# Kernel optimization log

Measured on AMD Instinct MI355X. Metric: run time of the kernel, lower is better.

## Reference

```python
import jax, jax.numpy as jnp
import numpy as np

# Contiguous token segment lengths per group (static, sums to 4096)
LEN_GROUPS = (256, 512, 768, 384, 640, 512, 576, 448)
NUM_GROUPS, D_IN, D_OUT = 8, 512, 512
BATCH = 16


def setup_inputs() -> dict:
    key = jax.random.key(0)
    k1, k2, k3 = jax.random.split(key, 3)
    T = int(sum(LEN_GROUPS))
    x = jax.random.normal(k1, (BATCH, T, D_IN), dtype=jnp.float32)
    # nn.Linear default init: U(-1/sqrt(fan_in), 1/sqrt(fan_in))
    bound = 1.0 / np.sqrt(D_IN)
    W = jax.random.uniform(k2, (NUM_GROUPS, D_OUT, D_IN), jnp.float32, -bound, bound)
    b = jax.random.uniform(k3, (NUM_GROUPS, D_OUT), jnp.float32, -bound, bound)
    return {"x": x, "W": W, "b": b}


def reference(x, W, b):
    # Per-group Linear over contiguous token segments, then concat along tokens.
    # Loop is over a small static group count; segment bounds are Python ints,
    # so slicing is static and jit-compatible.
    outs = []
    start = 0
    for i, L in enumerate(LEN_GROUPS):
        seg = x[:, start:start + L]                     # [B, L, D_in]
        outs.append(jnp.einsum('btd,od->bto', seg, W[i]) + b[i])  # [B, L, D_out]
        start += L
    return jnp.concatenate(outs, axis=1)               # [B, T, D_out]
```

## Files before the change

### kernel.cpp

```cpp
#include <hip/hip_runtime.h>
#include <hip/hip_bf16.h>
#include <cstdint>

#define BATCH 16
#define TTOT  4096
#define DIN   512
#define DOUT  512
#define NG    8
#define NJOB  33
#define NKT   16

typedef float f32x4 __attribute__((ext_vector_type(4)));
typedef short s16x8 __attribute__((ext_vector_type(8)));

__device__ __forceinline__ short f2b(float f) {
    union { __bf16 b; short s; } u; u.b = (__bf16)f; return u.s;
}

__device__ __constant__ short JT0[NJOB] = {
    0,128, 256,384,512,640, 768,896,1024,1152,1280,1408, 1536,1664,1792,
    1920,2048,2176,2304,2432, 2560,2688,2816,2944, 3072,3200,3328,3456,
    3584, 3648, 3712,3840,3968};
__device__ __constant__ char JG[NJOB] = {
    0,0, 1,1,1,1, 2,2,2,2,2,2, 3,3,3, 4,4,4,4,4, 5,5,5,5, 6,6,6,6, 6, 7, 7,7,7};
__device__ __constant__ char JBM[NJOB] = {
    127,127, 127,127,127,127, 127,127,127,127,127,127, 127,127,127,
    127,127,127,127,127, 127,127,127,127, 127,127,127,127, 63, 63, 127,127,127};

__global__ void wconv_kernel(const float* __restrict__ W, ushort* __restrict__ wbf) {
    int gid = blockIdx.x * 256 + threadIdx.x;
    int c = gid >> 9;
    int q = (gid & 511) << 4;
    int r = q >> 6;
    int slot = (q >> 4) & 3;
    int kt = c & 15, nt = (c >> 4) & 3, g = c >> 6;
    int k = (kt << 5) + (((slot ^ ((r >> 1) & 3))) << 3);
    const float* wp = W + ((size_t)((g << 9) + (nt << 7) + r) << 9) + k;
    float4 v0 = *reinterpret_cast<const float4*>(wp);
    float4 v1 = *reinterpret_cast<const float4*>(wp + 4);
    s16x8 o;
    o[0]=f2b(v0.x); o[1]=f2b(v0.y); o[2]=f2b(v0.z); o[3]=f2b(v0.w);
    o[4]=f2b(v1.x); o[5]=f2b(v1.y); o[6]=f2b(v1.z); o[7]=f2b(v1.w);
    *reinterpret_cast<s16x8*>((char*)wbf + (size_t)c * 8192 + q) = o;
}

__launch_bounds__(256, 4)
__global__ void gemm_kernel(const float* __restrict__ x,
                            const ushort* __restrict__ wbf,
                            const float* __restrict__ bias,
                            float* __restrict__ out) {
    __shared__ __align__(16) char smem[32768];

    const int tid  = threadIdx.x;
    const int lane = tid & 63;
    const int wv   = tid >> 6;
    const int wm   = wv >> 1;
    const int wn   = wv & 1;
    const int colf = lane & 15;
    const int kg   = lane >> 4;

    const int p    = blockIdx.x;
    const int l    = (p & 7) * 264 + (p >> 3);
    const int nt   = l & 3;
    const int rest = l >> 2;
    const int job  = rest >> 4;
    const int bb   = rest & 15;
    const int t0   = JT0[job];
    const int g    = JG[job];
    const int bmm1 = JBM[job];
    const int n0   = nt << 7;

    const char* bchunk = (const char*)wbf + ((size_t)(((g << 2) + nt) << 4)) * 8192;

    const int r = tid >> 1;
    const int h = tid & 1;
    const int re = (r <= bmm1) ? r : bmm1;
    const float* aptr = x + ((size_t)(bb * TTOT + t0 + re) << 9) + (h << 4);
    const int sr = (r >> 1) & 3;
    const int aw0 = (r << 6) + ((((h << 1) | 0) ^ sr) << 4);
    const int aw1 = (r << 6) + ((((h << 1) | 1) ^ sr) << 4);

    float4 aE[4], aO[4];

#define ISSUE_A(S, KT_) do {                                                \
        const float* p_ = aptr + ((KT_) << 5);                              \
        a##S[0] = *(const float4*)(p_);                                     \
        a##S[1] = *(const float4*)(p_ + 4);                                 \
        a##S[2] = *(const float4*)(p_ + 8);                                 \
        a##S[3] = *(const float4*)(p_ + 12);                                \
    } while (0)

#define CVT_WRITE_A(S, KT_) do {                                            \
        char* ab_ = smem + (((KT_) & 1) << 13);                             \
        s16x8 o0_, o1_;                                                     \
        o0_[0]=f2b(a##S[0].x); o0_[1]=f2b(a##S[0].y);                       \
        o0_[2]=f2b(a##S[0].z); o0_[3]=f2b(a##S[0].w);                       \
        o0_[4]=f2b(a##S[1].x); o0_[5]=f2b(a##S[1].y);                       \
        o0_[6]=f2b(a##S[1].z); o0_[7]=f2b(a##S[1].w);                       \
        o1_[0]=f2b(a##S[2].x); o1_[1]=f2b(a##S[2].y);                       \
        o1_[2]=f2b(a##S[2].z); o1_[3]=f2b(a##S[2].w);                       \
        o1_[4]=f2b(a##S[3].x); o1_[5]=f2b(a##S[3].y);                       \
        o1_[6]=f2b(a##S[3].z); o1_[7]=f2b(a##S[3].w);                       \
        *(s16x8*)(ab_ + aw0) = o0_;                                         \
        *(s16x8*)(ab_ + aw1) = o1_;                                         \
    } while (0)

#define ISSUE_B(KT_) do {                                                   \
        const char* s_ = bchunk + ((size_t)(KT_) << 13) + tid * 16;         \
        char* d_ = smem + 16384 + (((KT_) & 1) << 13) + tid * 16;           \
        __builtin_amdgcn_global_load_lds(                                   \
            (const __attribute__((address_space(1))) void*)(s_),            \
            (__attribute__((address_space(3))) void*)(d_), 16, 0, 0);       \
        __builtin_amdgcn_global_load_lds(                                   \
            (const __attribute__((address_space(1))) void*)(s_ + 4096),     \
            (__attribute__((address_space(3))) void*)(d_ + 4096), 16, 0, 0);\
    } while (0)

#define COMPUTE(KT_) do {                                                   \
        const char* ab_ = smem + (((KT_) & 1) << 13);                       \
        const char* bb_ = smem + 16384 + (((KT_) & 1) << 13);               \
        __builtin_amdgcn_s_setprio(1);                                      \
        s16x8 bf[4];                                                        \
        _Pragma("unroll")                                                   \
        for (int ni = 0; ni < 4; ++ni) {                                    \
            int r_ = wn * 64 + ni * 16 + colf;                              \
            bf[ni] = *(const s16x8*)(bb_ + (r_ << 6)                        \
                        + (((kg ^ ((r_ >> 1) & 3))) << 4));                 \
        }                                                                   \
        _Pragma("unroll")                                                   \
        for (int mi = 0; mi < 4; ++mi) {                                    \
            int r_ = wm * 64 + mi * 16 + colf;                              \
            s16x8 af = *(const s16x8*)(ab_ + (r_ << 6)                      \
                        + (((kg ^ ((r_ >> 1) & 3))) << 4));                 \
            _Pragma("unroll")                                               \
            for (int ni = 0; ni < 4; ++ni)                                  \
                acc[mi][ni] = __builtin_amdgcn_mfma_f32_16x16x32_bf16(      \
                    af, bf[ni], acc[mi][ni], 0, 0, 0);                      \
        }                                                                   \
        __builtin_amdgcn_s_setprio(0);                                      \
    } while (0)

#define FENCE  asm volatile("" ::: "memory")
#define WAITV4 asm volatile("s_waitcnt vmcnt(4)" ::: "memory")
#define WAITV0 asm volatile("s_waitcnt vmcnt(0)" ::: "memory")
#define WAITL0 asm volatile("s_waitcnt lgkmcnt(0)" ::: "memory")
#define BAR    __builtin_amdgcn_s_barrier()

    f32x4 acc[4][4];
#pragma unroll
    for (int mi = 0; mi < 4; ++mi)
#pragma unroll
        for (int ni = 0; ni < 4; ++ni)
            acc[mi][ni] = (f32x4){0.f, 0.f, 0.f, 0.f};

    ISSUE_A(E, 0);
    FENCE;
    ISSUE_B(0);
    FENCE;
    ISSUE_A(O, 1);
    FENCE;
    CVT_WRITE_A(E, 0);
    WAITV4;
    WAITL0;
    BAR;

#pragma unroll
    for (int kt = 0; kt < NKT; ++kt) {
        if (kt + 1 < NKT) { ISSUE_B(kt + 1); FENCE; }
        if (kt + 2 < NKT) {
            if (((kt + 2) & 1) == 0) { ISSUE_A(E, kt + 2); }
            else                     { ISSUE_A(O, kt + 2); }
            FENCE;
        }
        COMPUTE(kt);
        if (kt + 1 < NKT) {
            if (((kt + 1) & 1) == 0) { CVT_WRITE_A(E, kt + 1); }
            else                     { CVT_WRITE_A(O, kt + 1); }
            if (kt + 2 < NKT) { WAITV4; }
            else              { WAITV0; }
            WAITL0;
            BAR;
        }
    }
    BAR;

    float* cbuf = (float*)smem;
    const int er = tid >> 3;
    const int ec = (tid & 7) << 4;
    float4 bvv[4];
#pragma unroll
    for (int i = 0; i < 4; ++i)
        bvv[i] = *(const float4*)(bias + (g << 9) + n0 + ec + (i << 2));

#pragma unroll
    for (int pp = 0; pp < 4; ++pp) {
        if (wm == (pp >> 1)) {
#pragma unroll
            for (int m = 0; m < 2; ++m) {
                const int mi = (pp & 1) * 2 + m;
#pragma unroll
                for (int ni = 0; ni < 4; ++ni) {
                    const int base = (m * 16 + kg * 4) * 132 + wn * 64 + ni * 16 + colf;
                    f32x4 v = acc[mi][ni];
                    cbuf[base]       = v[0];
                    cbuf[base + 132] = v[1];
                    cbuf[base + 264] = v[2];
                    cbuf[base + 396] = v[3];
                }
            }
        }
        WAITL0;
        BAR;
        const int row = pp * 32 + er;
        if (row <= bmm1) {
            float* orow = out + ((size_t)(bb * TTOT + t0 + row) << 9) + n0 + ec;
            const float* crow = cbuf + er * 132 + ec;
#pragma unroll
            for (int i = 0; i < 4; ++i) {
                float4 v = *(const float4*)(crow + (i << 2));
                float4 o4;
                o4.x = v.x + bvv[i].x; o4.y = v.y + bvv[i].y;
                o4.z = v.z + bvv[i].z; o4.w = v.w + bvv[i].w;
                *(float4*)(orow + (i << 2)) = o4;
            }
        }
        BAR;
    }
#undef ISSUE_A
#undef CVT_WRITE_A
#undef ISSUE_B
#undef COMPUTE
#undef FENCE
#undef WAITV4
#undef WAITV0
#undef WAITL0
#undef BAR
}

__launch_bounds__(256)
__global__ void gemm_fallback(const float* __restrict__ x,
                              const float* __restrict__ W,
                              const float* __restrict__ bias,
                              float* __restrict__ out) {
    __shared__ __align__(16) char smem[49152];
    const int tid  = threadIdx.x;
    const int lane = tid & 63;
    const int wid  = tid >> 6;
    const int wm   = wid >> 1;
    const int wn   = wid & 1;
    const int p  = blockIdx.x;
    const int l  = ((p & 7) << 9) + (p >> 3);
    const int mt = l >> 2;
    const int nt = l & 3;
    const int bb = mt >> 6;
    const int t0 = (mt & 63) << 6;
    const int n0 = nt << 7;
    int g = 0;
    if (t0 >= 256)  g++; if (t0 >= 768)  g++; if (t0 >= 1536) g++;
    if (t0 >= 1920) g++; if (t0 >= 2560) g++; if (t0 >= 3072) g++;
    if (t0 >= 3648) g++;
    const int arow = tid >> 2;
    const int acol = (tid & 3) << 4;
    const float* aptr = x + ((size_t)(bb * TTOT + t0 + arow)) * DIN + acol;
    float4 a0, a1, a2, a3;
    float4 bw0[4], bw1[4];
    auto load_global = [&](int k0) {
        a0 = *(const float4*)(aptr + k0);
        a1 = *(const float4*)(aptr + k0 + 4);
        a2 = *(const float4*)(aptr + k0 + 8);
        a3 = *(const float4*)(aptr + k0 + 12);
#pragma unroll
        for (int pp = 0; pp < 4; ++pp) {
            int idx = pp * 256 + tid;
            int row = idx >> 3, seg = idx & 7;
            const float* wp = W + ((size_t)((g << 9) + n0 + row)) * DIN + k0 + (seg << 3);
            bw0[pp] = *(const float4*)(wp);
            bw1[pp] = *(const float4*)(wp + 4);
        }
    };
    auto swzf = [](int row, int bc) { return (row << 7) + (bc ^ ((row & 7) << 4)); };
    auto write_lds = [&](int buf) {
        char* ab  = smem + buf * 8192;
        char* bb_ = smem + 16384 + buf * 16384;
        s16x8 w0, w1;
        w0[0]=f2b(a0.x); w0[1]=f2b(a0.y); w0[2]=f2b(a0.z); w0[3]=f2b(a0.w);
        w0[4]=f2b(a1.x); w0[5]=f2b(a1.y); w0[6]=f2b(a1.z); w0[7]=f2b(a1.w);
        w1[0]=f2b(a2.x); w1[1]=f2b(a2.y); w1[2]=f2b(a2.z); w1[3]=f2b(a2.w);
        w1[4]=f2b(a3.x); w1[5]=f2b(a3.y); w1[6]=f2b(a3.z); w1[7]=f2b(a3.w);
        const int abase2 = acol << 1;
        *(s16x8*)(ab + swzf(arow, abase2))      = w0;
        *(s16x8*)(ab + swzf(arow, abase2 + 16)) = w1;
#pragma unroll
        for (int pp = 0; pp < 4; ++pp) {
            int idx = pp * 256 + tid;
            int row = idx >> 3, seg = idx & 7;
            s16x8 wvv;
            wvv[0]=f2b(bw0[pp].x); wvv[1]=f2b(bw0[pp].y);
            wvv[2]=f2b(bw0[pp].z); wvv[3]=f2b(bw0[pp].w);
            wvv[4]=f2b(bw1[pp].x); wvv[5]=f2b(bw1[pp].y);
            wvv[6]=f2b(bw1[pp].z); wvv[7]=f2b(bw1[pp].w);
            *(s16x8*)(bb_ + swzf(row, seg << 4)) = wvv;
        }
    };
    f32x4 acc[2][4];
#pragma unroll
    for (int mi = 0; mi < 2; ++mi)
#pragma unroll
        for (int ni = 0; ni < 4; ++ni) acc[mi][ni] = (f32x4){0.f,0.f,0.f,0.f};
    const int colf = lane & 15;
    const int kgrp = lane >> 4;
    auto compute = [&](int buf) {
        const char* ab  = smem + buf * 8192;
        const char* bb_ = smem + 16384 + buf * 16384;
#pragma unroll
        for (int ks = 0; ks < 2; ++ks) {
            const int kb = ks * 64 + kgrp * 16;
            s16x8 af[2], bf[4];
#pragma unroll
            for (int mi = 0; mi < 2; ++mi)
                af[mi] = *(const s16x8*)(ab + swzf(wm * 32 + mi * 16 + colf, kb));
#pragma unroll
            for (int ni = 0; ni < 4; ++ni)
                bf[ni] = *(const s16x8*)(bb_ + swzf(wn * 64 + ni * 16 + colf, kb));
#pragma unroll
            for (int mi = 0; mi < 2; ++mi)
#pragma unroll
                for (int ni = 0; ni < 4; ++ni)
                    acc[mi][ni] = __builtin_amdgcn_mfma_f32_16x16x32_bf16(
                        af[mi], bf[ni], acc[mi][ni], 0, 0, 0);
        }
    };
    load_global(0);
    write_lds(0);
    __syncthreads();
    int buf = 0;
#pragma unroll 1
    for (int kt = 0; kt < 8; ++kt) {
        if (kt < 7) load_global((kt + 1) << 6);
        compute(buf);
        if (kt < 7) write_lds(buf ^ 1);
        __syncthreads();
        buf ^= 1;
    }
    float* cbuf = (float*)smem;
#pragma unroll
    for (int ni = 0; ni < 4; ++ni) {
        const int c = wn * 64 + ni * 16 + colf;
#pragma unroll
        for (int mi = 0; mi < 2; ++mi) {
            const int rr2 = wm * 32 + mi * 16 + kgrp * 4;
            f32x4 v = acc[mi][ni];
            cbuf[(rr2 + 0) * 132 + c] = v[0];
            cbuf[(rr2 + 1) * 132 + c] = v[1];
            cbuf[(rr2 + 2) * 132 + c] = v[2];
            cbuf[(rr2 + 3) * 132 + c] = v[3];
        }
    }
    __syncthreads();
    const int rr = tid >> 5;
    const int cc = (tid & 31) << 2;
    const float4 bvv = *(const float4*)(bias + (g << 9) + n0 + cc);
#pragma unroll
    for (int it = 0; it < 8; ++it) {
        const int row = it * 8 + rr;
        float4 v = *(const float4*)(cbuf + row * 132 + cc);
        float4 o4; o4.x = v.x + bvv.x; o4.y = v.y + bvv.y;
                   o4.z = v.z + bvv.z; o4.w = v.w + bvv.w;
        *(float4*)(out + ((size_t)(bb * TTOT) + t0 + row) * DOUT + n0 + cc) = o4;
    }
}

extern "C" void kernel_launch(void* const* d_in, const int* in_sizes, int n_in,
                              void* d_out, int out_size, void* d_ws, size_t ws_size,
                              hipStream_t stream) {
    const float* x    = (const float*)d_in[0];
    const float* W    = (const float*)d_in[1];
    const float* bias = (const float*)d_in[2];
    float* out = (float*)d_out;

    const size_t wbytes = (size_t)NG * DOUT * DIN * sizeof(ushort);

    if (ws_size >= wbytes) {
        ushort* wbf = (ushort*)d_ws;
        wconv_kernel<<<1024, 256, 0, stream>>>(W, wbf);
        gemm_kernel<<<NJOB * BATCH * 4, 256, 0, stream>>>(x, wbf, bias, out);
    } else {
        gemm_fallback<<<BATCH * 64 * 4, 256, 0, stream>>>(x, W, bias, out);
    }
}
```

Measured before the change: 117.0 us.

## Load pre-swizzled weight fragments straight into registers and double the K tile

The weight conversion now writes bf16 W in MFMA fragment order, so each wave loads its B operands straight from global memory into registers instead of staging them through LDS with global_load_lds. The K tile doubles to 64, halving the number of k-steps and barriers. The A tile gets a new 128-byte-row XOR swizzle in a 32 KB double buffer. The aim is to free LDS bandwidth and cut synchronisation, at the cost of more live registers, so launch bounds drop to 2 blocks per CU and latency hiding may suffer.

New measurement: 102.5 us. -12.4%, faster.

```diff
diff --git a/kernel.cpp b/kernel.cpp
--- a/kernel.cpp
+++ b/kernel.cpp
@@ -8,7 +8,7 @@
 #define DOUT  512
 #define NG    8
 #define NJOB  33
-#define NKT   16
+#define NKT   8
 
 typedef float f32x4 __attribute__((ext_vector_type(4)));
 typedef short s16x8 __attribute__((ext_vector_type(8)));
@@ -29,22 +29,26 @@
 
 __global__ void wconv_kernel(const float* __restrict__ W, ushort* __restrict__ wbf) {
     int gid = blockIdx.x * 256 + threadIdx.x;
-    int c = gid >> 9;
-    int q = (gid & 511) << 4;
-    int r = q >> 6;
-    int slot = (q >> 4) & 3;
-    int kt = c & 15, nt = (c >> 4) & 3, g = c >> 6;
-    int k = (kt << 5) + (((slot ^ ((r >> 1) & 3))) << 3);
-    const float* wp = W + ((size_t)((g << 9) + (nt << 7) + r) << 9) + k;
+    int l  = gid & 63;
+    int u  = gid >> 6;
+    int ks = u & 1;
+    int ni = (u >> 1) & 3;
+    int wn = (u >> 3) & 1;
+    int kt = (u >> 4) & 7;
+    int nt = (u >> 7) & 3;
+    int g  = u >> 9;
+    int row = nt * 128 + wn * 64 + ni * 16 + (l & 15);
+    int k   = kt * 64 + ks * 32 + (l >> 4) * 8;
+    const float* wp = W + ((size_t)(g * DOUT + row)) * DIN + k;
     float4 v0 = *reinterpret_cast<const float4*>(wp);
     float4 v1 = *reinterpret_cast<const float4*>(wp + 4);
     s16x8 o;
     o[0]=f2b(v0.x); o[1]=f2b(v0.y); o[2]=f2b(v0.z); o[3]=f2b(v0.w);
     o[4]=f2b(v1.x); o[5]=f2b(v1.y); o[6]=f2b(v1.z); o[7]=f2b(v1.w);
-    *reinterpret_cast<s16x8*>((char*)wbf + (size_t)c * 8192 + q) = o;
-}
-
-__launch_bounds__(256, 4)
+    *reinterpret_cast<s16x8*>((char*)wbf + (size_t)gid * 16) = o;
+}
+
+__launch_bounds__(256, 2)
 __global__ void gemm_kernel(const float* __restrict__ x,
                             const ushort* __restrict__ wbf,
                             const float* __restrict__ bias,
@@ -70,79 +74,67 @@
     const int bmm1 = JBM[job];
     const int n0   = nt << 7;
 
-    const char* bchunk = (const char*)wbf + ((size_t)(((g << 2) + nt) << 4)) * 8192;
-
-    const int r = tid >> 1;
-    const int h = tid & 1;
-    const int re = (r <= bmm1) ? r : bmm1;
-    const float* aptr = x + ((size_t)(bb * TTOT + t0 + re) << 9) + (h << 4);
-    const int sr = (r >> 1) & 3;
-    const int aw0 = (r << 6) + ((((h << 1) | 0) ^ sr) << 4);
-    const int aw1 = (r << 6) + ((((h << 1) | 1) ^ sr) << 4);
-
-    float4 aE[4], aO[4];
+    const char* bfbase = (const char*)wbf
+        + ((size_t)((g * 4 + nt) * 8)) * 16384 + (wn ? 8192 : 0) + lane * 16;
+
+    const int arow_s = (wv << 5) + (lane >> 3);
+    const int col8   = (lane & 7) << 3;
+    const float* aptr = x + ((size_t)(bb * TTOT + t0 + arow_s)) * DIN + col8;
+
+    float4 stE[4][2], stO[4][2];
+    s16x8 bE[8], bO[8];
 
 #define ISSUE_A(S, KT_) do {                                                \
-        const float* p_ = aptr + ((KT_) << 5);                              \
-        a##S[0] = *(const float4*)(p_);                                     \
-        a##S[1] = *(const float4*)(p_ + 4);                                 \
-        a##S[2] = *(const float4*)(p_ + 8);                                 \
-        a##S[3] = *(const float4*)(p_ + 12);                                \
+        _Pragma("unroll")                                                   \
+        for (int j_ = 0; j_ < 4; ++j_) {                                    \
+            const float* p_ = aptr + (size_t)(j_ * 8) * DIN + ((KT_) << 6); \
+            st##S[j_][0] = *(const float4*)(p_);                            \
+            st##S[j_][1] = *(const float4*)(p_ + 4);                        \
+        }                                                                   \
     } while (0)
 
 #define CVT_WRITE_A(S, KT_) do {                                            \
-        char* ab_ = smem + (((KT_) & 1) << 13);                             \
-        s16x8 o0_, o1_;                                                     \
-        o0_[0]=f2b(a##S[0].x); o0_[1]=f2b(a##S[0].y);                       \
-        o0_[2]=f2b(a##S[0].z); o0_[3]=f2b(a##S[0].w);                       \
-        o0_[4]=f2b(a##S[1].x); o0_[5]=f2b(a##S[1].y);                       \
-        o0_[6]=f2b(a##S[1].z); o0_[7]=f2b(a##S[1].w);                       \
-        o1_[0]=f2b(a##S[2].x); o1_[1]=f2b(a##S[2].y);                       \
-        o1_[2]=f2b(a##S[2].z); o1_[3]=f2b(a##S[2].w);                       \
-        o1_[4]=f2b(a##S[3].x); o1_[5]=f2b(a##S[3].y);                       \
-        o1_[6]=f2b(a##S[3].z); o1_[7]=f2b(a##S[3].w);                       \
-        *(s16x8*)(ab_ + aw0) = o0_;                                         \
-        *(s16x8*)(ab_ + aw1) = o1_;                                         \
+        char* ab_ = smem + (((KT_) & 1) << 14);                             \
+        _Pragma("unroll")                                                   \
+        for (int j_ = 0; j_ < 4; ++j_) {                                    \
+            float4 lo_ = st##S[j_][0], hi_ = st##S[j_][1];                  \
+            s16x8 o_;                                                       \
+            o_[0]=f2b(lo_.x); o_[1]=f2b(lo_.y); o_[2]=f2b(lo_.z); o_[3]=f2b(lo_.w); \
+            o_[4]=f2b(hi_.x); o_[5]=f2b(hi_.y); o_[6]=f2b(hi_.z); o_[7]=f2b(hi_.w); \
+            int row_ = arow_s + j_ * 8;                                     \
+            int bc_ = (col8 << 1) ^ ((row_ & 7) << 4);                      \
+            *(s16x8*)(ab_ + (row_ << 7) + bc_) = o_;                        \
+        }                                                                   \
     } while (0)
 
-#define ISSUE_B(KT_) do {                                                   \
-        const char* s_ = bchunk + ((size_t)(KT_) << 13) + tid * 16;         \
-        char* d_ = smem + 16384 + (((KT_) & 1) << 13) + tid * 16;           \
-        __builtin_amdgcn_global_load_lds(                                   \
-            (const __attribute__((address_space(1))) void*)(s_),            \
-            (__attribute__((address_space(3))) void*)(d_), 16, 0, 0);       \
-        __builtin_amdgcn_global_load_lds(                                   \
-            (const __attribute__((address_space(1))) void*)(s_ + 4096),     \
-            (__attribute__((address_space(3))) void*)(d_ + 4096), 16, 0, 0);\
+#define ISSUE_BF(S, KT_) do {                                               \
+        const char* b_ = bfbase + ((size_t)(KT_) << 14);                    \
+        _Pragma("unroll")                                                   \
+        for (int q_ = 0; q_ < 8; ++q_)                                      \
+            b##S[q_] = *(const s16x8*)(b_ + q_ * 1024);                     \
     } while (0)
 
-#define COMPUTE(KT_) do {                                                   \
-        const char* ab_ = smem + (((KT_) & 1) << 13);                       \
-        const char* bb_ = smem + 16384 + (((KT_) & 1) << 13);               \
-        __builtin_amdgcn_s_setprio(1);                                      \
-        s16x8 bf[4];                                                        \
+#define COMPUTE(S, KT_) do {                                                \
+        const char* ab_ = smem + (((KT_) & 1) << 14);                       \
         _Pragma("unroll")                                                   \
-        for (int ni = 0; ni < 4; ++ni) {                                    \
-            int r_ = wn * 64 + ni * 16 + colf;                              \
-            bf[ni] = *(const s16x8*)(bb_ + (r_ << 6)                        \
-                        + (((kg ^ ((r_ >> 1) & 3))) << 4));                 \
+        for (int ks = 0; ks < 2; ++ks) {                                    \
+            const int kb = ks * 64 + (kg << 4);                             \
+            s16x8 af[4];                                                    \
+            _Pragma("unroll")                                               \
+            for (int mi = 0; mi < 4; ++mi) {                                \
+                int r_ = wm * 64 + mi * 16 + colf;                          \
+                af[mi] = *(const s16x8*)(ab_ + (r_ << 7) + (kb ^ ((r_ & 7) << 4))); \
+            }                                                               \
+            _Pragma("unroll")                                               \
+            for (int mi = 0; mi < 4; ++mi)                                  \
+                _Pragma("unroll")                                           \
+                for (int ni = 0; ni < 4; ++ni)                              \
+                    acc[mi][ni] = __builtin_amdgcn_mfma_f32_16x16x32_bf16(  \
+                        af[mi], b##S[ni * 2 + ks], acc[mi][ni], 0, 0, 0);   \
         }                                                                   \
-        _Pragma("unroll")                                                   \
-        for (int mi = 0; mi < 4; ++mi) {                                    \
-            int r_ = wm * 64 + mi * 16 + colf;                              \
-            s16x8 af = *(const s16x8*)(ab_ + (r_ << 6)                      \
-                        + (((kg ^ ((r_ >> 1) & 3))) << 4));                 \
-            _Pragma("unroll")                                               \
-            for (int ni = 0; ni < 4; ++ni)                                  \
-                acc[mi][ni] = __builtin_amdgcn_mfma_f32_16x16x32_bf16(      \
-                    af, bf[ni], acc[mi][ni], 0, 0, 0);                      \
-        }                                                                   \
-        __builtin_amdgcn_s_setprio(0);                                      \
     } while (0)
 
 #define FENCE  asm volatile("" ::: "memory")
-#define WAITV4 asm volatile("s_waitcnt vmcnt(4)" ::: "memory")
-#define WAITV0 asm volatile("s_waitcnt vmcnt(0)" ::: "memory")
 #define WAITL0 asm volatile("s_waitcnt lgkmcnt(0)" ::: "memory")
 #define BAR    __builtin_amdgcn_s_barrier()
 
@@ -153,31 +145,31 @@
         for (int ni = 0; ni < 4; ++ni)
             acc[mi][ni] = (f32x4){0.f, 0.f, 0.f, 0.f};
 
+    ISSUE_BF(E, 0);
     ISSUE_A(E, 0);
-    FENCE;
-    ISSUE_B(0);
     FENCE;
     ISSUE_A(O, 1);
     FENCE;
     CVT_WRITE_A(E, 0);
-    WAITV4;
     WAITL0;
     BAR;
 
 #pragma unroll
     for (int kt = 0; kt < NKT; ++kt) {
-        if (kt + 1 < NKT) { ISSUE_B(kt + 1); FENCE; }
+        if (kt + 1 < NKT) {
+            if (((kt + 1) & 1) == 0) { ISSUE_BF(E, kt + 1); }
+            else                     { ISSUE_BF(O, kt + 1); }
+            FENCE;
+        }
         if (kt + 2 < NKT) {
             if (((kt + 2) & 1) == 0) { ISSUE_A(E, kt + 2); }
             else                     { ISSUE_A(O, kt + 2); }
             FENCE;
         }
-        COMPUTE(kt);
+        if ((kt & 1) == 0) { COMPUTE(E, kt); } else { COMPUTE(O, kt); }
         if (kt + 1 < NKT) {
             if (((kt + 1) & 1) == 0) { CVT_WRITE_A(E, kt + 1); }
             else                     { CVT_WRITE_A(O, kt + 1); }
-            if (kt + 2 < NKT) { WAITV4; }
-            else              { WAITV0; }
             WAITL0;
             BAR;
         }
@@ -213,7 +205,7 @@
         BAR;
         const int row = pp * 32 + er;
         if (row <= bmm1) {
-            float* orow = out + ((size_t)(bb * TTOT + t0 + row) << 9) + n0 + ec;
+            float* orow = out + ((size_t)(bb * TTOT + t0 + row)) * DOUT + n0 + ec;
             const float* crow = cbuf + er * 132 + ec;
 #pragma unroll
             for (int i = 0; i < 4; ++i) {
@@ -228,11 +220,9 @@
     }
 #undef ISSUE_A
 #undef CVT_WRITE_A
-#undef ISSUE_B
+#undef ISSUE_BF
 #undef COMPUTE
 #undef FENCE
-#undef WAITV4
-#undef WAITV0
 #undef WAITL0
 #undef BAR
 }
```

## Load fp32 A tiles directly into LDS and use three-stage async pipeline

Applied to the files above, without the earlier changes.

A tiles are now loaded as fp32 straight into LDS with global_load_lds instead of going through registers and a bf16 conversion before the LDS write. Conversion to bf16 moves into the compute step, applied when fragments are read from LDS. The double buffer becomes a three-slot ring, prefetching two stages ahead with vmcnt(6). This removes register staging and the per-iteration LDS write and lgkm wait. In exchange LDS grows to 72KB, occupancy bounds drop from 4 to 2 blocks, and A-tile LDS traffic doubles because the data stays fp32.

Result: faster. 101.4 us (-13.3%).

```diff
diff --git a/kernel.cpp b/kernel.cpp
--- a/kernel.cpp
+++ b/kernel.cpp
@@ -44,12 +44,12 @@
     *reinterpret_cast<s16x8*>((char*)wbf + (size_t)c * 8192 + q) = o;
 }
 
-__launch_bounds__(256, 4)
+__launch_bounds__(256, 2)
 __global__ void gemm_kernel(const float* __restrict__ x,
                             const ushort* __restrict__ wbf,
                             const float* __restrict__ bias,
                             float* __restrict__ out) {
-    __shared__ __align__(16) char smem[32768];
+    __shared__ __align__(16) char smem[73728];
 
     const int tid  = threadIdx.x;
     const int lane = tid & 63;
@@ -72,76 +72,70 @@
 
     const char* bchunk = (const char*)wbf + ((size_t)(((g << 2) + nt) << 4)) * 8192;
 
-    const int r = tid >> 1;
-    const int h = tid & 1;
-    const int re = (r <= bmm1) ? r : bmm1;
-    const float* aptr = x + ((size_t)(bb * TTOT + t0 + re) << 9) + (h << 4);
-    const int sr = (r >> 1) & 3;
-    const int aw0 = (r << 6) + ((((h << 1) | 0) ^ sr) << 4);
-    const int aw1 = (r << 6) + ((((h << 1) | 1) ^ sr) << 4);
-
-    float4 aE[4], aO[4];
-
-#define ISSUE_A(S, KT_) do {                                                \
-        const float* p_ = aptr + ((KT_) << 5);                              \
-        a##S[0] = *(const float4*)(p_);                                     \
-        a##S[1] = *(const float4*)(p_ + 4);                                 \
-        a##S[2] = *(const float4*)(p_ + 8);                                 \
-        a##S[3] = *(const float4*)(p_ + 12);                                \
+    const int srcslot = ((tid & 7) ^ ((tid >> 3) & 7)) << 4;
+    const char* pA0; const char* pA1; const char* pA2; const char* pA3;
+    {
+        int r0 = (tid >> 3);
+        int r1 = 32 + r0, r2 = 64 + r0, r3 = 96 + r0;
+        if (r2 > bmm1) r2 -= 64;
+        if (r3 > bmm1) r3 -= 64;
+        const char* xb = (const char*)(x + ((size_t)(bb * TTOT + t0)) * DIN);
+        pA0 = xb + (size_t)r0 * 2048 + srcslot;
+        pA1 = xb + (size_t)r1 * 2048 + srcslot;
+        pA2 = xb + (size_t)r2 * 2048 + srcslot;
+        pA3 = xb + (size_t)r3 * 2048 + srcslot;
+    }
+
+#define GLD(SRC_, DST_)                                                     \
+    __builtin_amdgcn_global_load_lds(                                       \
+        (const __attribute__((address_space(1))) void*)(SRC_),              \
+        (__attribute__((address_space(3))) void*)(DST_), 16, 0, 0)
+
+#define STAGE(KT_, SL_) do {                                                \
+        char* sb_ = smem + (SL_) * 24576;                                   \
+        GLD(pA0 + (KT_) * 128, sb_ + tid * 16);                             \
+        GLD(pA1 + (KT_) * 128, sb_ + 4096  + tid * 16);                     \
+        GLD(pA2 + (KT_) * 128, sb_ + 8192  + tid * 16);                     \
+        GLD(pA3 + (KT_) * 128, sb_ + 12288 + tid * 16);                     \
+        const char* bs_ = bchunk + (size_t)(KT_) * 8192 + tid * 16;         \
+        GLD(bs_,        sb_ + 16384 + tid * 16);                            \
+        GLD(bs_ + 4096, sb_ + 20480 + tid * 16);                            \
     } while (0)
 
-#define CVT_WRITE_A(S, KT_) do {                                            \
-        char* ab_ = smem + (((KT_) & 1) << 13);                             \
-        s16x8 o0_, o1_;                                                     \
-        o0_[0]=f2b(a##S[0].x); o0_[1]=f2b(a##S[0].y);                       \
-        o0_[2]=f2b(a##S[0].z); o0_[3]=f2b(a##S[0].w);                       \
-        o0_[4]=f2b(a##S[1].x); o0_[5]=f2b(a##S[1].y);                       \
-        o0_[6]=f2b(a##S[1].z); o0_[7]=f2b(a##S[1].w);                       \
-        o1_[0]=f2b(a##S[2].x); o1_[1]=f2b(a##S[2].y);                       \
-        o1_[2]=f2b(a##S[2].z); o1_[3]=f2b(a##S[2].w);                       \
-        o1_[4]=f2b(a##S[3].x); o1_[5]=f2b(a##S[3].y);                       \
-        o1_[6]=f2b(a##S[3].z); o1_[7]=f2b(a##S[3].w);                       \
-        *(s16x8*)(ab_ + aw0) = o0_;                                         \
-        *(s16x8*)(ab_ + aw1) = o1_;                                         \
-    } while (0)
-
-#define ISSUE_B(KT_) do {                                                   \
-        const char* s_ = bchunk + ((size_t)(KT_) << 13) + tid * 16;         \
-        char* d_ = smem + 16384 + (((KT_) & 1) << 13) + tid * 16;           \
-        __builtin_amdgcn_global_load_lds(                                   \
-            (const __attribute__((address_space(1))) void*)(s_),            \
-            (__attribute__((address_space(3))) void*)(d_), 16, 0, 0);       \
-        __builtin_amdgcn_global_load_lds(                                   \
-            (const __attribute__((address_space(1))) void*)(s_ + 4096),     \
-            (__attribute__((address_space(3))) void*)(d_ + 4096), 16, 0, 0);\
-    } while (0)
-
-#define COMPUTE(KT_) do {                                                   \
-        const char* ab_ = smem + (((KT_) & 1) << 13);                       \
-        const char* bb_ = smem + 16384 + (((KT_) & 1) << 13);               \
+#define COMPUTE(KT_, SL_) do {                                              \
+        const char* ab_ = smem + (SL_) * 24576;                             \
+        const char* bb_ = ab_ + 16384;                                      \
         __builtin_amdgcn_s_setprio(1);                                      \
         s16x8 bf[4];                                                        \
         _Pragma("unroll")                                                   \
         for (int ni = 0; ni < 4; ++ni) {                                    \
             int r_ = wn * 64 + ni * 16 + colf;                              \
             bf[ni] = *(const s16x8*)(bb_ + (r_ << 6)                        \
-                        + (((kg ^ ((r_ >> 1) & 3))) << 4));                 \
+                        + ((kg ^ ((r_ >> 1) & 3)) << 4));                   \
         }                                                                   \
         _Pragma("unroll")                                                   \
         for (int mi = 0; mi < 4; ++mi) {                                    \
             int r_ = wm * 64 + mi * 16 + colf;                              \
-            s16x8 af = *(const s16x8*)(ab_ + (r_ << 6)                      \
-                        + (((kg ^ ((r_ >> 1) & 3))) << 4));                 \
+            const char* base_ = ab_ + (r_ << 7);                            \
+            int s0_ = ((kg << 1) ^ (r_ & 7)) << 4;                          \
+            int s1_ = (((kg << 1) | 1) ^ (r_ & 7)) << 4;                    \
+            f32x4 lo_ = *(const f32x4*)(base_ + s0_);                       \
+            f32x4 hi_ = *(const f32x4*)(base_ + s1_);                       \
+            s16x8 af_;                                                      \
+            af_[0]=f2b(lo_[0]); af_[1]=f2b(lo_[1]);                         \
+            af_[2]=f2b(lo_[2]); af_[3]=f2b(lo_[3]);                         \
+            af_[4]=f2b(hi_[0]); af_[5]=f2b(hi_[1]);                         \
+            af_[6]=f2b(hi_[2]); af_[7]=f2b(hi_[3]);                         \
             _Pragma("unroll")                                               \
             for (int ni = 0; ni < 4; ++ni)                                  \
                 acc[mi][ni] = __builtin_amdgcn_mfma_f32_16x16x32_bf16(      \
-                    af, bf[ni], acc[mi][ni], 0, 0, 0);                      \
+                    af_, bf[ni], acc[mi][ni], 0, 0, 0);                     \
         }                                                                   \
         __builtin_amdgcn_s_setprio(0);                                      \
     } while (0)
 
 #define FENCE  asm volatile("" ::: "memory")
-#define WAITV4 asm volatile("s_waitcnt vmcnt(4)" ::: "memory")
+#define WAITV6 asm volatile("s_waitcnt vmcnt(6)" ::: "memory")
 #define WAITV0 asm volatile("s_waitcnt vmcnt(0)" ::: "memory")
 #define WAITL0 asm volatile("s_waitcnt lgkmcnt(0)" ::: "memory")
 #define BAR    __builtin_amdgcn_s_barrier()
@@ -153,32 +147,20 @@
         for (int ni = 0; ni < 4; ++ni)
             acc[mi][ni] = (f32x4){0.f, 0.f, 0.f, 0.f};
 
-    ISSUE_A(E, 0);
+    STAGE(0, 0);
     FENCE;
-    ISSUE_B(0);
+    STAGE(1, 1);
     FENCE;
-    ISSUE_A(O, 1);
-    FENCE;
-    CVT_WRITE_A(E, 0);
-    WAITV4;
-    WAITL0;
+    WAITV6;
     BAR;
 
 #pragma unroll
     for (int kt = 0; kt < NKT; ++kt) {
-        if (kt + 1 < NKT) { ISSUE_B(kt + 1); FENCE; }
-        if (kt + 2 < NKT) {
-            if (((kt + 2) & 1) == 0) { ISSUE_A(E, kt + 2); }
-            else                     { ISSUE_A(O, kt + 2); }
-            FENCE;
-        }
-        COMPUTE(kt);
-        if (kt + 1 < NKT) {
-            if (((kt + 1) & 1) == 0) { CVT_WRITE_A(E, kt + 1); }
-            else                     { CVT_WRITE_A(O, kt + 1); }
-            if (kt + 2 < NKT) { WAITV4; }
+        if (kt + 2 < NKT) { STAGE(kt + 2, (kt + 2) % 3); FENCE; }
+        COMPUTE(kt, kt % 3);
+        if (kt < NKT - 1) {
+            if (kt < NKT - 2) { WAITV6; }
             else              { WAITV0; }
-            WAITL0;
             BAR;
         }
     }
@@ -213,7 +195,7 @@
         BAR;
         const int row = pp * 32 + er;
         if (row <= bmm1) {
-            float* orow = out + ((size_t)(bb * TTOT + t0 + row) << 9) + n0 + ec;
+            float* orow = out + ((size_t)(bb * TTOT + t0 + row)) * DOUT + n0 + ec;
             const float* crow = cbuf + er * 132 + ec;
 #pragma unroll
             for (int i = 0; i < 4; ++i) {
@@ -226,12 +208,11 @@
         }
         BAR;
     }
-#undef ISSUE_A
-#undef CVT_WRITE_A
-#undef ISSUE_B
+#undef GLD
+#undef STAGE
 #undef COMPUTE
 #undef FENCE
-#undef WAITV4
+#undef WAITV6
 #undef WAITV0
 #undef WAITL0
 #undef BAR
```
